# Kernel optimization log

Hardware: AMD Instinct MI355X
Metric: run time of the kernel (lower is better)

Reference implementation:

```python
import jax, jax.numpy as jnp
import numpy as np

D_MODEL = 1024
NUM_HEADS = 16
D_K = D_MODEL // NUM_HEADS


def setup_inputs() -> dict:
    key = jax.random.key(0)
    ks = jax.random.split(key, 9)
    s = 1.0 / np.sqrt(D_MODEL)
    x = jax.random.normal(ks[0], (4, 2048, D_MODEL), dtype=jnp.float32)
    Wq = jax.random.uniform(ks[1], (D_MODEL, D_MODEL), jnp.float32, -s, s)
    bq = jax.random.uniform(ks[2], (D_MODEL,), jnp.float32, -s, s)
    Wk = jax.random.uniform(ks[3], (D_MODEL, D_MODEL), jnp.float32, -s, s)
    bk = jax.random.uniform(ks[4], (D_MODEL,), jnp.float32, -s, s)
    Wv = jax.random.uniform(ks[5], (D_MODEL, D_MODEL), jnp.float32, -s, s)
    bv = jax.random.uniform(ks[6], (D_MODEL,), jnp.float32, -s, s)
    Wo = jax.random.uniform(ks[7], (D_MODEL, D_MODEL), jnp.float32, -s, s)
    bo = jax.random.uniform(ks[8], (D_MODEL,), jnp.float32, -s, s)
    return {"x": x, "Wq": Wq, "bq": bq, "Wk": Wk, "bk": bk,
            "Wv": Wv, "bv": bv, "Wo": Wo, "bo": bo}


def reference(x, Wq, bq, Wk, bk, Wv, bv, Wo, bo):
    B, T, C = x.shape
    H, Dk = NUM_HEADS, D_K
    # linear projections (torch Linear: x @ W.T + b; here W stored as [in,out])
    q = (x @ Wq + bq).reshape(B, T, H, Dk).transpose(0, 2, 1, 3)  # [B,H,T,Dk]
    k = (x @ Wk + bk).reshape(B, T, H, Dk).transpose(0, 2, 1, 3)
    v = (x @ Wv + bv).reshape(B, T, H, Dk).transpose(0, 2, 1, 3)
    scores = jnp.einsum("bhtd,bhsd->bhts", q, k) / jnp.sqrt(jnp.float32(Dk))
    attn = jax.nn.softmax(scores, axis=-1)  # [B,H,T,T]
    context = jnp.einsum("bhts,bhsd->bhtd", attn, v)
    context = context.transpose(0, 2, 1, 3).reshape(B, T, C)
    return context @ Wo + bo
```

## Files before the change

### kernel.cpp

```cpp
#include <hip/hip_runtime.h>
#include <hip/hip_bf16.h>
#include <stdint.h>

typedef short bf16x8 __attribute__((ext_vector_type(8)));
typedef short bf16x4 __attribute__((ext_vector_type(4)));
typedef float f32x4  __attribute__((ext_vector_type(4)));

#define MFMA16(a, b, c) __builtin_amdgcn_mfma_f32_16x16x32_bf16((a), (b), (c), 0, 0, 0)

__device__ __forceinline__ unsigned short f2bf(float f) {
    union { float f; unsigned int u; } v; v.f = f;
    unsigned int u = v.u;
    u += 0x7fffu + ((u >> 16) & 1u);
    return (unsigned short)(u >> 16);
}

__device__ __forceinline__ unsigned int trunc_pk(float a, float b) {
    return (__float_as_uint(a) >> 16) | (__float_as_uint(b) & 0xffff0000u);
}

__device__ __forceinline__ float exp2f_fast(float x) {
#if __has_builtin(__builtin_amdgcn_exp2f)
    return __builtin_amdgcn_exp2f(x);
#else
    return exp2f(x);
#endif
}

__device__ __forceinline__ void g2lds16(const void* g, void* l) {
    __builtin_amdgcn_global_load_lds(
        (const __attribute__((address_space(1))) void*)g,
        (__attribute__((address_space(3))) void*)l, 16, 0, 0);
}


__global__ __launch_bounds__(256) void convert_x_kernel(
    const float4* __restrict__ src, ushort4* __restrict__ dst)
{
    int i = blockIdx.x * 256 + threadIdx.x;
    float4 v = src[i];
    ushort4 o;
    o.x = f2bf(v.x); o.y = f2bf(v.y); o.z = f2bf(v.z); o.w = f2bf(v.w);
    dst[i] = o;
}

__global__ __launch_bounds__(256) void transpose_w4_kernel(
    const float* __restrict__ W0, const float* __restrict__ W1,
    const float* __restrict__ W2, const float* __restrict__ W3,
    unsigned short* __restrict__ dst_base)
{
    __shared__ float tile[64][65];
    const int z = blockIdx.z;
    const float* src = (z == 0) ? W0 : (z == 1) ? W1 : (z == 2) ? W2 : W3;
    unsigned short* dst = dst_base + ((size_t)z << 20);
    const int k0 = blockIdx.x * 64, n0 = blockIdx.y * 64;
    const int tx = threadIdx.x & 63, ty = threadIdx.x >> 6;
    #pragma unroll
    for (int i = 0; i < 64; i += 4)
        tile[ty + i][tx] = src[(size_t)(k0 + ty + i) * 1024 + n0 + tx];
    __syncthreads();
    #pragma unroll
    for (int i = 0; i < 64; i += 4)
        dst[(size_t)(n0 + ty + i) * 1024 + k0 + tx] = f2bf(tile[tx][ty + i]);
}


#define QSCALE 0.18033688011112042f

template <int MODE>
__global__ __launch_bounds__(256, 2) void gemm_bt(
    const unsigned short* __restrict__ A, const unsigned short* __restrict__ Bt,
    const float* __restrict__ b0, const float* __restrict__ b1, const float* __restrict__ b2,
    unsigned short* __restrict__ Qb, unsigned short* __restrict__ Kb,
    unsigned short* __restrict__ Vt, float* __restrict__ out)
{
    __shared__ alignas(16) unsigned short As[2][2][128 * 32];
    __shared__ alignas(16) unsigned short Bs[2][2][128 * 32];

    const int t = threadIdx.x;
    const int m0 = blockIdx.y * 128, n0 = blockIdx.x * 128;
    const int lane = t & 63, w = t >> 6, quad = lane >> 4, c16 = lane & 15;
    const int moff = (w >> 1) * 64, noff = (w & 1) * 64;

    f32x4 acc[4][4];
    #pragma unroll
    for (int i = 0; i < 4; ++i)
        #pragma unroll
        for (int j = 0; j < 4; ++j)
            acc[i][j] = (f32x4){0.f, 0.f, 0.f, 0.f};

    const unsigned short* Ag = A + (size_t)(m0 + (t >> 2)) * 1024 + (t & 3) * 8;
    const unsigned short* Bg = Bt + (size_t)(n0 + (t >> 2)) * 1024 + (t & 3) * 8;
    unsigned short* Asl = &As[0][0][0] + t * 8;
    unsigned short* Bsl = &Bs[0][0][0] + t * 8;

#define STAGE(bufv, k0v)                                                    \
    do {                                                                    \
        unsigned short* Ad = Asl + (bufv) * 8192;                           \
        unsigned short* Bd = Bsl + (bufv) * 8192;                           \
        g2lds16(Ag + (k0v),                  Ad);                           \
        g2lds16(Ag + (k0v) + 32,             Ad + 4096);                    \
        g2lds16(Ag + 64 * 1024 + (k0v),      Ad + 2048);                    \
        g2lds16(Ag + 64 * 1024 + (k0v) + 32, Ad + 4096 + 2048);             \
        g2lds16(Bg + (k0v),                  Bd);                           \
        g2lds16(Bg + (k0v) + 32,             Bd + 4096);                    \
        g2lds16(Bg + 64 * 1024 + (k0v),      Bd + 2048);                    \
        g2lds16(Bg + 64 * 1024 + (k0v) + 32, Bd + 4096 + 2048);             \
    } while (0)

    STAGE(0, 0);

    for (int kt = 0; kt < 16; ++kt) {
        const int buf = kt & 1;
        if (kt < 15) {
            STAGE(buf ^ 1, (kt + 1) * 64);
            asm volatile("s_waitcnt vmcnt(8)" ::: "memory");
        } else {
            asm volatile("s_waitcnt vmcnt(0)" ::: "memory");
        }
        __builtin_amdgcn_sched_barrier(0);
        __builtin_amdgcn_s_barrier();
        __builtin_amdgcn_sched_barrier(0);

        #pragma unroll
        for (int kk = 0; kk < 2; ++kk) {
            const unsigned short* Ab = &As[buf][kk][0];
            const unsigned short* Bb = &Bs[buf][kk][0];
            bf16x8 af[4], bfr[4];
            #pragma unroll
            for (int ms = 0; ms < 4; ++ms)
                af[ms] = *(const bf16x8*)(Ab + (moff + ms * 16 + c16) * 32 + quad * 8);
            #pragma unroll
            for (int ns = 0; ns < 4; ++ns)
                bfr[ns] = *(const bf16x8*)(Bb + (noff + ns * 16 + c16) * 32 + quad * 8);
            #pragma unroll
            for (int ms = 0; ms < 4; ++ms)
                #pragma unroll
                for (int ns = 0; ns < 4; ++ns)
                    acc[ms][ns] = MFMA16(af[ms], bfr[ns], acc[ms][ns]);
        }

        if (kt < 15) {
            asm volatile("s_waitcnt lgkmcnt(0)" ::: "memory");
            __builtin_amdgcn_sched_barrier(0);
            __builtin_amdgcn_s_barrier();
            __builtin_amdgcn_sched_barrier(0);
        }
    }
#undef STAGE

    #pragma unroll
    for (int ns = 0; ns < 4; ++ns) {
        const int n = n0 + noff + ns * 16 + c16;
        if (MODE == 0) {
            const int mat = n >> 10, nn = n & 1023;
            const int h = nn >> 6, d = nn & 63;
            const float bias = (mat == 0) ? b0[nn] : ((mat == 1) ? b1[nn] : b2[nn]);
            #pragma unroll
            for (int ms = 0; ms < 4; ++ms) {
                const int mbase = m0 + moff + ms * 16 + quad * 4;
                const int b = mbase >> 11, tbase = mbase & 2047;
                const int bh = b * 16 + h;
                if (mat == 2) {
                    ushort4 pk;
                    pk.x = f2bf(acc[ms][ns][0] + bias);
                    pk.y = f2bf(acc[ms][ns][1] + bias);
                    pk.z = f2bf(acc[ms][ns][2] + bias);
                    pk.w = f2bf(acc[ms][ns][3] + bias);
                    *(ushort4*)(Vt + ((size_t)bh * 64 + d) * 2048 + tbase) = pk;
                } else {
                    #pragma unroll
                    for (int r = 0; r < 4; ++r) {
                        float v = acc[ms][ns][r] + bias;
                        if (mat == 0) v *= QSCALE;
                        unsigned short* dst = (mat == 0) ? Qb : Kb;
                        dst[((size_t)bh * 2048 + tbase + r) * 64 + d] = f2bf(v);
                    }
                }
            }
        } else {
            const float bias = b0[n];
            #pragma unroll
            for (int ms = 0; ms < 4; ++ms) {
                #pragma unroll
                for (int r = 0; r < 4; ++r) {
                    const int m = m0 + moff + ms * 16 + quad * 4 + r;
                    out[(size_t)m * 1024 + n] = acc[ms][ns][r] + bias;
                }
            }
        }
    }
}


__global__ __launch_bounds__(256, 4) void attn_kernel(
    const unsigned short* __restrict__ Qb, const unsigned short* __restrict__ Kb,
    const unsigned short* __restrict__ Vt, unsigned short* __restrict__ ctx)
{
    __shared__ alignas(16) unsigned short Ks[2][64 * 64];
    __shared__ alignas(16) unsigned short Vs[2][64 * 64];

    const int t = threadIdx.x, w = t >> 6, lane = t & 63;
    const int quad = lane >> 4, c16 = lane & 15;
    const int L = blockIdx.y * 16 + blockIdx.x;
    const int bh = ((L & 7) << 3) + (L >> 7);
    const int qt = (L >> 3) & 15;
    const int qbase = qt * 128 + w * 32;

    bf16x8 qf[2][2];
    #pragma unroll
    for (int mt = 0; mt < 2; ++mt) {
        const unsigned short* Qp = Qb + ((size_t)bh * 2048 + qbase + mt * 16 + c16) * 64;
        qf[mt][0] = *(const bf16x8*)(Qp + quad * 8);
        qf[mt][1] = *(const bf16x8*)(Qp + 32 + quad * 8);
    }

    float l_r[2] = {0.f, 0.f};
    f32x4 O[2][4];
    #pragma unroll
    for (int mt = 0; mt < 2; ++mt)
        #pragma unroll
        for (int dc = 0; dc < 4; ++dc) O[mt][dc] = (f32x4){0.f, 0.f, 0.f, 0.f};

    const int sgrp = (t & 7) ^ ((t >> 3) & 7);
    const unsigned short* Kgl = Kb + (size_t)bh * 131072 + (size_t)(t >> 3) * 64 + sgrp * 8;
    const unsigned short* Vgl = Vt + (size_t)bh * 131072 + (size_t)(t >> 3) * 2048 + sgrp * 8;
    const int tOff = t * 8;
    const f32x4 fzero = {0.f, 0.f, 0.f, 0.f};

    #pragma unroll
    for (int q = 0; q < 2; ++q) {
        g2lds16(Kgl + q * 2048,  Ks[0] + tOff + q * 2048);
        g2lds16(Vgl + (size_t)q * 65536, Vs[0] + tOff + q * 2048);
    }

    for (int it = 0; it < 32; ++it) {
        const int cur = it & 1;
        const unsigned short* Kc = Ks[cur];
        const unsigned short* Vc = Vs[cur];

        if (it < 31) {
            const int s0 = (it + 1) * 64;
            unsigned short* Kn = Ks[cur ^ 1] + tOff;
            unsigned short* Vn = Vs[cur ^ 1] + tOff;
            #pragma unroll
            for (int q = 0; q < 2; ++q) {
                g2lds16(Kgl + (size_t)s0 * 64 + q * 2048,    Kn + q * 2048);
                g2lds16(Vgl + s0 + (size_t)q * 65536,        Vn + q * 2048);
            }
            asm volatile("s_waitcnt vmcnt(4)" ::: "memory");
        } else {
            asm volatile("s_waitcnt vmcnt(0)" ::: "memory");
        }
        __builtin_amdgcn_sched_barrier(0);
        __builtin_amdgcn_s_barrier();
        __builtin_amdgcn_sched_barrier(0);

        #pragma unroll
        for (int ctp = 0; ctp < 2; ++ctp) {
            union { bf16x8 v; unsigned int d[4]; } af8[2];
            union { bf16x8 v; uint2 u[2]; } v8[4];

            #pragma unroll
            for (int ct2 = 0; ct2 < 2; ++ct2) {
                const int ct = ctp * 2 + ct2;
                const int key = ct * 16 + c16;
                const bf16x8 kf0 = *(const bf16x8*)(Kc + key * 64 + ((quad ^ (key & 7)) << 3));
                const bf16x8 kf1 = *(const bf16x8*)(Kc + key * 64 + (((4 + quad) ^ (key & 7)) << 3));

                const int g = ct * 2 + (quad >> 1);
                #pragma unroll
                for (int dc = 0; dc < 4; ++dc) {
                    const int d = dc * 16 + c16;
                    v8[dc].u[ct2] = *(const uint2*)(Vc + d * 64 + ((g ^ (d & 7)) << 3) + (quad & 1) * 4);
                }

                #pragma unroll
                for (int mt = 0; mt < 2; ++mt) {
                    f32x4 sa = MFMA16(kf0, qf[mt][0], fzero);
                    sa = MFMA16(kf1, qf[mt][1], sa);
                    const float p0 = exp2f_fast(sa[0]);
                    const float p1 = exp2f_fast(sa[1]);
                    const float p2 = exp2f_fast(sa[2]);
                    const float p3 = exp2f_fast(sa[3]);
                    l_r[mt] += (p0 + p1) + (p2 + p3);
                    af8[mt].d[ct2 * 2 + 0] = trunc_pk(p0, p1);
                    af8[mt].d[ct2 * 2 + 1] = trunc_pk(p2, p3);
                }
            }

            #pragma unroll
            for (int mt = 0; mt < 2; ++mt)
                #pragma unroll
                for (int dc = 0; dc < 4; ++dc)
                    O[mt][dc] = MFMA16(af8[mt].v, v8[dc].v, O[mt][dc]);
        }

        if (it < 31) {
            asm volatile("s_waitcnt lgkmcnt(0)" ::: "memory");
            __builtin_amdgcn_sched_barrier(0);
            __builtin_amdgcn_s_barrier();
            __builtin_amdgcn_sched_barrier(0);
        }
    }

    #pragma unroll
    for (int mt = 0; mt < 2; ++mt) {
        l_r[mt] += __shfl_xor(l_r[mt], 16);
        l_r[mt] += __shfl_xor(l_r[mt], 32);
    }

    const int b = bh >> 4, h = bh & 15;
    #pragma unroll
    for (int mt = 0; mt < 2; ++mt) {
        float inv[4];
        #pragma unroll
        for (int r = 0; r < 4; ++r)
            inv[r] = 1.0f / __shfl(l_r[mt], quad * 4 + r);
        #pragma unroll
        for (int dc = 0; dc < 4; ++dc)
            #pragma unroll
            for (int r = 0; r < 4; ++r) {
                const int row = qbase + mt * 16 + quad * 4 + r;
                ctx[((size_t)(b * 2048 + row)) * 1024 + h * 64 + dc * 16 + c16] =
                    f2bf(O[mt][dc][r] * inv[r]);
            }
    }
}


extern "C" void kernel_launch(void* const* d_in, const int* in_sizes, int n_in,
                              void* d_out, int out_size, void* d_ws, size_t ws_size,
                              hipStream_t stream)
{
    const float* x  = (const float*)d_in[0];
    const float* Wq = (const float*)d_in[1];
    const float* bq = (const float*)d_in[2];
    const float* Wk = (const float*)d_in[3];
    const float* bk = (const float*)d_in[4];
    const float* Wv = (const float*)d_in[5];
    const float* bv = (const float*)d_in[6];
    const float* Wo = (const float*)d_in[7];
    const float* bo = (const float*)d_in[8];
    float* out = (float*)d_out;

    char* ws = (char*)d_ws;
    unsigned short* xb    = (unsigned short*)(ws);
    unsigned short* Wqkvt = (unsigned short*)(ws + (16u << 20));
    unsigned short* Vt    = (unsigned short*)(ws + (24u << 20));
    unsigned short* Wot   = Wqkvt + (3u << 20);
    unsigned short* Qb    = (unsigned short*)((char*)d_out);
    unsigned short* Kb    = (unsigned short*)((char*)d_out + (16u << 20));

    convert_x_kernel<<<8192, 256, 0, stream>>>((const float4*)x, (ushort4*)xb);
    transpose_w4_kernel<<<dim3(16, 16, 4), 256, 0, stream>>>(Wq, Wk, Wv, Wo, Wqkvt);

    gemm_bt<0><<<dim3(24, 64), 256, 0, stream>>>(xb, Wqkvt, bq, bk, bv, Qb, Kb, Vt, nullptr);
    attn_kernel<<<dim3(16, 64), 256, 0, stream>>>(Qb, Kb, Vt, xb );
    gemm_bt<1><<<dim3(8, 64), 256, 0, stream>>>(xb, Wot, bo, nullptr, nullptr,
                                                nullptr, nullptr, nullptr, out);
}
```

Measured before the change: 278.2 us.

## Triple-buffer K/V tiles in LDS and drop the trailing per-iteration barrier

Grows the K and V shared-memory ring in the attention kernel from two to three stages and rotates buffer pointers each iteration. With a free slot between the tile being read and the tile being written, the end-of-iteration lgkmcnt wait and workgroup barrier can be removed. The swizzled LDS offsets for K and V fragments are also precomputed outside the loop. In exchange, LDS per block goes up by half and launch bounds drop to 3 blocks per CU. With 1024 blocks, that risks a second partial wave of blocks and lower latency hiding.

Result: no change. 283.7 us (+2.0%).

```diff
diff --git a/kernel.cpp b/kernel.cpp
--- a/kernel.cpp
+++ b/kernel.cpp
@@ -193,12 +193,12 @@
 }
 
 
-__global__ __launch_bounds__(256, 4) void attn_kernel(
+__global__ __launch_bounds__(256, 3) void attn_kernel(
     const unsigned short* __restrict__ Qb, const unsigned short* __restrict__ Kb,
     const unsigned short* __restrict__ Vt, unsigned short* __restrict__ ctx)
 {
-    __shared__ alignas(16) unsigned short Ks[2][64 * 64];
-    __shared__ alignas(16) unsigned short Vs[2][64 * 64];
+    __shared__ alignas(16) unsigned short Ks[3][64 * 64];
+    __shared__ alignas(16) unsigned short Vs[3][64 * 64];
 
     const int t = threadIdx.x, w = t >> 6, lane = t & 63;
     const int quad = lane >> 4, c16 = lane & 15;
@@ -222,31 +222,37 @@
         #pragma unroll
         for (int dc = 0; dc < 4; ++dc) O[mt][dc] = (f32x4){0.f, 0.f, 0.f, 0.f};
 
+    const int kb0 = c16 * 64 + ((quad ^ (c16 & 7)) << 3);
+    const int kb1 = c16 * 64 + (((4 + quad) ^ (c16 & 7)) << 3);
+    int voff[4];
+    #pragma unroll
+    for (int ct = 0; ct < 4; ++ct)
+        voff[ct] = c16 * 64 + (((ct * 2 + (quad >> 1)) ^ (c16 & 7)) << 3) + (quad & 1) * 4;
+
     const int sgrp = (t & 7) ^ ((t >> 3) & 7);
     const unsigned short* Kgl = Kb + (size_t)bh * 131072 + (size_t)(t >> 3) * 64 + sgrp * 8;
     const unsigned short* Vgl = Vt + (size_t)bh * 131072 + (size_t)(t >> 3) * 2048 + sgrp * 8;
     const int tOff = t * 8;
     const f32x4 fzero = {0.f, 0.f, 0.f, 0.f};
 
+    const unsigned short *Kc = Ks[0], *Ka = Ks[1], *Kb2 = Ks[2];
+    const unsigned short *V0 = Vs[0], *Va = Vs[1], *Vb2 = Vs[2];
+
     #pragma unroll
     for (int q = 0; q < 2; ++q) {
-        g2lds16(Kgl + q * 2048,  Ks[0] + tOff + q * 2048);
-        g2lds16(Vgl + (size_t)q * 65536, Vs[0] + tOff + q * 2048);
+        g2lds16(Kgl + q * 2048,          (unsigned short*)Kc + tOff + q * 2048);
+        g2lds16(Vgl + (size_t)q * 65536, (unsigned short*)V0 + tOff + q * 2048);
     }
 
     for (int it = 0; it < 32; ++it) {
-        const int cur = it & 1;
-        const unsigned short* Kc = Ks[cur];
-        const unsigned short* Vc = Vs[cur];
-
         if (it < 31) {
             const int s0 = (it + 1) * 64;
-            unsigned short* Kn = Ks[cur ^ 1] + tOff;
-            unsigned short* Vn = Vs[cur ^ 1] + tOff;
+            unsigned short* Kn = (unsigned short*)Ka + tOff;
+            unsigned short* Vn = (unsigned short*)Va + tOff;
             #pragma unroll
             for (int q = 0; q < 2; ++q) {
-                g2lds16(Kgl + (size_t)s0 * 64 + q * 2048,    Kn + q * 2048);
-                g2lds16(Vgl + s0 + (size_t)q * 65536,        Vn + q * 2048);
+                g2lds16(Kgl + (size_t)s0 * 64 + q * 2048, Kn + q * 2048);
+                g2lds16(Vgl + s0 + (size_t)q * 65536,     Vn + q * 2048);
             }
             asm volatile("s_waitcnt vmcnt(4)" ::: "memory");
         } else {
@@ -264,16 +270,12 @@
             #pragma unroll
             for (int ct2 = 0; ct2 < 2; ++ct2) {
                 const int ct = ctp * 2 + ct2;
-                const int key = ct * 16 + c16;
-                const bf16x8 kf0 = *(const bf16x8*)(Kc + key * 64 + ((quad ^ (key & 7)) << 3));
-                const bf16x8 kf1 = *(const bf16x8*)(Kc + key * 64 + (((4 + quad) ^ (key & 7)) << 3));
-
-                const int g = ct * 2 + (quad >> 1);
-                #pragma unroll
-                for (int dc = 0; dc < 4; ++dc) {
-                    const int d = dc * 16 + c16;
-                    v8[dc].u[ct2] = *(const uint2*)(Vc + d * 64 + ((g ^ (d & 7)) << 3) + (quad & 1) * 4);
-                }
+                const bf16x8 kf0 = *(const bf16x8*)(Kc + kb0 + ct * 1024);
+                const bf16x8 kf1 = *(const bf16x8*)(Kc + kb1 + ct * 1024);
+
+                #pragma unroll
+                for (int dc = 0; dc < 4; ++dc)
+                    v8[dc].u[ct2] = *(const uint2*)(V0 + voff[ct] + dc * 1024);
 
                 #pragma unroll
                 for (int mt = 0; mt < 2; ++mt) {
@@ -296,12 +298,8 @@
                     O[mt][dc] = MFMA16(af8[mt].v, v8[dc].v, O[mt][dc]);
         }
 
-        if (it < 31) {
-            asm volatile("s_waitcnt lgkmcnt(0)" ::: "memory");
-            __builtin_amdgcn_sched_barrier(0);
-            __builtin_amdgcn_s_barrier();
-            __builtin_amdgcn_sched_barrier(0);
-        }
+        const unsigned short* tk = Kc; Kc = Ka; Ka = Kb2; Kb2 = tk;
+        const unsigned short* tv = V0; V0 = Va; Va = Vb2; Vb2 = tv;
     }
 
     #pragma unroll
```

## Enlarge GEMM tiles to 256x128 with 512 threads, XOR-swizzled LDS, interleaved prefetch

Applied to the files above, without the earlier changes.

The projection GEMMs move from 128x128 tiles with 256 threads to 256x128 tiles with 512 threads (8 waves). The shared-memory layout becomes 64-wide rows with an XOR swizzle to avoid bank conflicts. Prefetch of the next K-tile is split across the two half-steps and interleaved with fragment loads, and MFMA priority is raised via setprio. This aims to improve B-operand reuse and cut LDS conflicts, but it uses more LDS per block and adds barriers per half-step, which may reduce occupancy.

After: 277.0 us. No clear change (-0.4%).

```diff
diff --git a/kernel.cpp b/kernel.cpp
--- a/kernel.cpp
+++ b/kernel.cpp
@@ -68,19 +68,20 @@
 #define QSCALE 0.18033688011112042f
 
 template <int MODE>
-__global__ __launch_bounds__(256, 2) void gemm_bt(
+__global__ __launch_bounds__(512, 2) void gemm256(
     const unsigned short* __restrict__ A, const unsigned short* __restrict__ Bt,
     const float* __restrict__ b0, const float* __restrict__ b1, const float* __restrict__ b2,
     unsigned short* __restrict__ Qb, unsigned short* __restrict__ Kb,
     unsigned short* __restrict__ Vt, float* __restrict__ out)
 {
-    __shared__ alignas(16) unsigned short As[2][2][128 * 32];
-    __shared__ alignas(16) unsigned short Bs[2][2][128 * 32];
+    __shared__ alignas(16) unsigned short As[2][256 * 64];
+    __shared__ alignas(16) unsigned short Bs[2][128 * 64];
 
     const int t = threadIdx.x;
-    const int m0 = blockIdx.y * 128, n0 = blockIdx.x * 128;
+    const int m0 = blockIdx.y * 256, n0 = blockIdx.x * 128;
     const int lane = t & 63, w = t >> 6, quad = lane >> 4, c16 = lane & 15;
-    const int moff = (w >> 1) * 64, noff = (w & 1) * 64;
+    const int moff = (w >> 1) * 64;
+    const int noff = (w & 1) * 64;
 
     f32x4 acc[4][4];
     #pragma unroll
@@ -89,65 +90,77 @@
         for (int j = 0; j < 4; ++j)
             acc[i][j] = (f32x4){0.f, 0.f, 0.f, 0.f};
 
-    const unsigned short* Ag = A + (size_t)(m0 + (t >> 2)) * 1024 + (t & 3) * 8;
-    const unsigned short* Bg = Bt + (size_t)(n0 + (t >> 2)) * 1024 + (t & 3) * 8;
-    unsigned short* Asl = &As[0][0][0] + t * 8;
-    unsigned short* Bsl = &Bs[0][0][0] + t * 8;
-
-#define STAGE(bufv, k0v)                                                    \
-    do {                                                                    \
-        unsigned short* Ad = Asl + (bufv) * 8192;                           \
-        unsigned short* Bd = Bsl + (bufv) * 8192;                           \
-        g2lds16(Ag + (k0v),                  Ad);                           \
-        g2lds16(Ag + (k0v) + 32,             Ad + 4096);                    \
-        g2lds16(Ag + 64 * 1024 + (k0v),      Ad + 2048);                    \
-        g2lds16(Ag + 64 * 1024 + (k0v) + 32, Ad + 4096 + 2048);             \
-        g2lds16(Bg + (k0v),                  Bd);                           \
-        g2lds16(Bg + (k0v) + 32,             Bd + 4096);                    \
-        g2lds16(Bg + 64 * 1024 + (k0v),      Bd + 2048);                    \
-        g2lds16(Bg + 64 * 1024 + (k0v) + 32, Bd + 4096 + 2048);             \
-    } while (0)
-
-    STAGE(0, 0);
+    const int sg = (t & 7) ^ ((t >> 3) & 7);
+    const unsigned short* Agl = A  + (size_t)(m0 + (t >> 3)) * 1024 + sg * 8;
+    const unsigned short* Bgl = Bt + (size_t)(n0 + (t >> 3)) * 1024 + sg * 8;
+    unsigned short* Asl = &As[0][0] + t * 8;
+    unsigned short* Bsl = &Bs[0][0] + t * 8;
+
+    #pragma unroll
+    for (int q = 0; q < 4; ++q)
+        g2lds16(Agl + (size_t)q * 65536, Asl + q * 4096);
+    #pragma unroll
+    for (int q = 0; q < 2; ++q)
+        g2lds16(Bgl + (size_t)q * 65536, Bsl + q * 4096);
+    asm volatile("s_waitcnt vmcnt(0)" ::: "memory");
+    __builtin_amdgcn_sched_barrier(0);
+    __builtin_amdgcn_s_barrier();
+    __builtin_amdgcn_sched_barrier(0);
+
+    const int swz = c16 & 7;
 
     for (int kt = 0; kt < 16; ++kt) {
         const int buf = kt & 1;
-        if (kt < 15) {
-            STAGE(buf ^ 1, (kt + 1) * 64);
-            asm volatile("s_waitcnt vmcnt(8)" ::: "memory");
-        } else {
-            asm volatile("s_waitcnt vmcnt(0)" ::: "memory");
-        }
-        __builtin_amdgcn_sched_barrier(0);
-        __builtin_amdgcn_s_barrier();
-        __builtin_amdgcn_sched_barrier(0);
-
-        #pragma unroll
-        for (int kk = 0; kk < 2; ++kk) {
-            const unsigned short* Ab = &As[buf][kk][0];
-            const unsigned short* Bb = &Bs[buf][kk][0];
+        const unsigned short* Ab = &As[buf][0];
+        const unsigned short* Bb = &Bs[buf][0];
+        unsigned short* An = Asl + (buf ^ 1) * 16384;
+        unsigned short* Bn = Bsl + (buf ^ 1) * 8192;
+        const size_t knext = (size_t)(kt + 1) * 64;
+
+        #pragma unroll
+        for (int kh = 0; kh < 2; ++kh) {
+            const int fgr = ((kh * 4 + quad) ^ swz) << 3;
             bf16x8 af[4], bfr[4];
             #pragma unroll
             for (int ms = 0; ms < 4; ++ms)
-                af[ms] = *(const bf16x8*)(Ab + (moff + ms * 16 + c16) * 32 + quad * 8);
+                af[ms] = *(const bf16x8*)(Ab + (moff + ms * 16 + c16) * 64 + fgr);
             #pragma unroll
             for (int ns = 0; ns < 4; ++ns)
-                bfr[ns] = *(const bf16x8*)(Bb + (noff + ns * 16 + c16) * 32 + quad * 8);
+                bfr[ns] = *(const bf16x8*)(Bb + (noff + ns * 16 + c16) * 64 + fgr);
+
+            if (kt < 15) {
+                if (kh == 0) {
+                    g2lds16(Agl + knext,                      An);
+                    g2lds16(Agl + knext + 65536,              An + 4096);
+                    g2lds16(Bgl + knext,                      Bn);
+                } else {
+                    g2lds16(Agl + knext + 2 * 65536,          An + 2 * 4096);
+                    g2lds16(Agl + knext + 3 * 65536,          An + 3 * 4096);
+                    g2lds16(Bgl + knext + 65536,              Bn + 4096);
+                }
+            }
+
+            __builtin_amdgcn_sched_barrier(0);
+            __builtin_amdgcn_s_barrier();
+            asm volatile("s_waitcnt lgkmcnt(0)" ::: "memory");
+            __builtin_amdgcn_sched_barrier(0);
+
+            __builtin_amdgcn_s_setprio(1);
             #pragma unroll
             for (int ms = 0; ms < 4; ++ms)
                 #pragma unroll
                 for (int ns = 0; ns < 4; ++ns)
                     acc[ms][ns] = MFMA16(af[ms], bfr[ns], acc[ms][ns]);
-        }
-
-        if (kt < 15) {
-            asm volatile("s_waitcnt lgkmcnt(0)" ::: "memory");
+            __builtin_amdgcn_s_setprio(0);
+
+            if (kh == 1) {
+                asm volatile("s_waitcnt vmcnt(0)" ::: "memory");
+            }
             __builtin_amdgcn_sched_barrier(0);
             __builtin_amdgcn_s_barrier();
             __builtin_amdgcn_sched_barrier(0);
         }
     }
-#undef STAGE
 
     #pragma unroll
     for (int ns = 0; ns < 4; ++ns) {
@@ -355,8 +368,8 @@
     convert_x_kernel<<<8192, 256, 0, stream>>>((const float4*)x, (ushort4*)xb);
     transpose_w4_kernel<<<dim3(16, 16, 4), 256, 0, stream>>>(Wq, Wk, Wv, Wo, Wqkvt);
 
-    gemm_bt<0><<<dim3(24, 64), 256, 0, stream>>>(xb, Wqkvt, bq, bk, bv, Qb, Kb, Vt, nullptr);
+    gemm256<0><<<dim3(24, 32), 512, 0, stream>>>(xb, Wqkvt, bq, bk, bv, Qb, Kb, Vt, nullptr);
     attn_kernel<<<dim3(16, 64), 256, 0, stream>>>(Qb, Kb, Vt, xb );
-    gemm_bt<1><<<dim3(8, 64), 256, 0, stream>>>(xb, Wot, bo, nullptr, nullptr,
+    gemm256<1><<<dim3(8, 32), 512, 0, stream>>>(xb, Wot, bo, nullptr, nullptr,
                                                 nullptr, nullptr, nullptr, out);
 }
```
